# Performance work log

Hardware: AMD Instinct MI355X
Metric: run time of the kernel (lower is better)

The kernel has to match this reference:

```python
import math
import jax, jax.numpy as jnp
import numpy as np

B, H, S, D = 2, 16, 2048, 64


def setup_inputs() -> dict:
    key = jax.random.key(0)
    kq, kk, kv = jax.random.split(key, 3)
    Q = jax.random.normal(kq, (B, H, S, D), dtype=jnp.float32)
    K = jax.random.normal(kk, (B, H, S, D), dtype=jnp.float32)
    V = jax.random.normal(kv, (B, H, S, D), dtype=jnp.float32)
    # padding mask: (N, H, query_len), True = keep (module expands with [..., None])
    padding_mask = jnp.ones((B, H, S), dtype=bool)
    # boolean causal attention mask, broadcastable to (B, H, S, S)
    attention_mask = jnp.tril(jnp.ones((S, S), dtype=bool))[None, None]
    return {"Q": Q, "K": K, "V": V,
            "padding_mask": padding_mask, "attention_mask": attention_mask}


def reference(Q, K, V, padding_mask, attention_mask):
    # scores: (B, H, S_q, S_k)
    scale = 1.0 / math.sqrt(K.shape[-1])
    attn = jnp.einsum("bhqd,bhkd->bhqk", Q, K) * scale
    # query-side padding mask (is_query_mask=True): expand last axis
    attn = jnp.where(padding_mask[..., None], attn, -jnp.inf)
    # boolean attention mask
    attn = jnp.where(attention_mask, attn, -jnp.inf)
    attn = jax.nn.softmax(attn, axis=-1)
    # nan-clean: rows fully masked to -inf softmax to NaN -> 0
    attn = jnp.where(jnp.isnan(attn), 0.0, attn)
    return jnp.einsum("bhqk,bhkd->bhqd", attn, V)
```

## Files before the change

kernel.cpp:

```cpp
#include <hip/hip_runtime.h>


typedef __attribute__((ext_vector_type(8))) short bf16x8;
typedef __attribute__((ext_vector_type(4))) float f32x4;
typedef __attribute__((ext_vector_type(4))) short s16x4;
typedef __attribute__((ext_vector_type(2))) unsigned uint2v;

#define MFMA16(a, b, c) __builtin_amdgcn_mfma_f32_16x16x32_bf16(a, b, c, 0, 0, 0)

#define S_LEN 2048
#define D_DIM 64
#define NBH 32

static __device__ __forceinline__ short f2bf(float f) {
  unsigned u = __builtin_bit_cast(unsigned, f);
  u += 0x7fffu + ((u >> 16) & 1u);
  return (short)(u >> 16);
}

static __device__ __forceinline__ unsigned pk2(float a, float b) {
#if __has_builtin(__builtin_amdgcn_cvt_pk_bf16_f32)
  auto r = __builtin_amdgcn_cvt_pk_bf16_f32(a, b);
  return __builtin_bit_cast(unsigned, r);
#else
  return (unsigned)(unsigned short)f2bf(a) |
         ((unsigned)(unsigned short)f2bf(b) << 16);
#endif
}

static __device__ __forceinline__ float fexp2(float x) {
#if __has_builtin(__builtin_amdgcn_exp2f)
  return __builtin_amdgcn_exp2f(x);
#else
  return exp2f(x);
#endif
}

static __device__ __forceinline__ bf16x8 cvt8(const float* p) {
  f32x4 a = *(const f32x4*)p;
  f32x4 b = *(const f32x4*)(p + 4);
  bf16x8 r;
#pragma unroll
  for (int j = 0; j < 4; ++j) { r[j] = f2bf(a[j]); r[j + 4] = f2bf(b[j]); }
  return r;
}

static __device__ __forceinline__ void load_lds16(const short* g, short* l) {
  __builtin_amdgcn_global_load_lds(
      (const __attribute__((address_space(1))) unsigned*)g,
      (__attribute__((address_space(3))) unsigned*)l, 16, 0, 0);
}

__global__ __launch_bounds__(256) void stage(const float* __restrict__ K,
                                             const float* __restrict__ V,
                                             short* __restrict__ Kb,
                                             short* __restrict__ Vt) {
  const int tid = threadIdx.x;
  if (blockIdx.x < 1024) {
    const size_t b0 = (size_t)blockIdx.x * 4096;
#pragma unroll
    for (int p = 0; p < 2; ++p) {
      const size_t i = b0 + p * 2048 + tid * 8;
      f32x4 a = *(const f32x4*)(K + i);
      f32x4 b = *(const f32x4*)(K + i + 4);
      bf16x8 r;
#pragma unroll
      for (int j = 0; j < 4; ++j) { r[j] = f2bf(a[j]); r[j + 4] = f2bf(b[j]); }
      *(bf16x8*)(Kb + i) = r;
    }
  } else {
    __shared__ unsigned t[64][18];
    const int bi = blockIdx.x - 1024;
    const int bh = bi >> 6, k32 = bi & 63;
    const float* src = V + ((size_t)bh * S_LEN + k32 * 32) * D_DIM;
    const int pr = tid & 15;
    const int dq = tid >> 4;
    f32x4 a = *(const f32x4*)(src + (2 * pr)     * D_DIM + dq * 4);
    f32x4 b = *(const f32x4*)(src + (2 * pr + 1) * D_DIM + dq * 4);
#pragma unroll
    for (int j = 0; j < 4; ++j) t[dq * 4 + j][pr] = pk2(a[j], b[j]);
    __syncthreads();
    const int d = tid >> 2, seg = tid & 3;
    uint2v lo = *(const uint2v*)(&t[d][seg * 4]);
    uint2v hi = *(const uint2v*)(&t[d][seg * 4 + 2]);
    short* dst = Vt + (size_t)bh * D_DIM * S_LEN + (size_t)d * S_LEN +
                 k32 * 32 + seg * 8;
    *(uint2v*)(dst)     = lo;
    *(uint2v*)(dst + 4) = hi;
  }
}

__global__ __launch_bounds__(256, 4) void attn_fwd(
    const float* __restrict__ Q, const short* __restrict__ Kb,
    const short* __restrict__ Vt, float* __restrict__ O) {
  __shared__ __align__(16) short kbuf[2][4096];
  __shared__ __align__(16) short vbuf[2][4096];
  __shared__ __align__(16) short pbuf[4][1024];

  const int tid  = threadIdx.x;
  const int wave = tid >> 6;
  const int lane = tid & 63;
  const int quad = lane >> 4;
  const int col  = lane & 15;

  const int bh = blockIdx.x & 31;
  const int qb = 31 - (blockIdx.x >> 5);
  const int n  = qb + 1;
  const int q0 = qb * 64 + wave * 16;

  const float* Qh = Q  + (size_t)bh * S_LEN * D_DIM;
  const short* Kh = Kb + (size_t)bh * S_LEN * D_DIM;
  const short* Vh = Vt + (size_t)bh * D_DIM * S_LEN;

  const bf16x8 bq0 = cvt8(Qh + (q0 + col) * D_DIM + quad * 8);
  const bf16x8 bq1 = cvt8(Qh + (q0 + col) * D_DIM + quad * 8 + 32);

  const int L0 = tid,       r0s = L0 >> 3, c0s = (L0 & 7) ^ (r0s & 7);
  const int L1 = 256 + tid, r1s = L1 >> 3, c1s = (L1 & 7) ^ (r1s & 7);
  const int wb0 = (wave * 64) * 8;
  const int wb1 = (256 + wave * 64) * 8;

  f32x4 o[4];
#pragma unroll
  for (int i = 0; i < 4; ++i) o[i] = 0.f;
  float psum = 0.f;
  const float sc = 0.125f * 1.44269504088896340736f;

  const int rbase = col * 64;
  const int sw0 = ((quad       ^ (col & 7)) << 3);
  const int sw1 = (((4 + quad) ^ (col & 7)) << 3);
  short* pw = &pbuf[wave][col * 64];
  const int cw0 = (quad >> 1), ho = (quad & 1) << 2;

  auto prefetch = [&](int t, int buf) {
    const int k0n = t << 6;
    load_lds16(Kh + (size_t)(k0n + r0s) * 64 + c0s * 8, &kbuf[buf][wb0]);
    load_lds16(Kh + (size_t)(k0n + r1s) * 64 + c1s * 8, &kbuf[buf][wb1]);
    load_lds16(Vh + (size_t)r0s * S_LEN + k0n + c0s * 8, &vbuf[buf][wb0]);
    load_lds16(Vh + (size_t)r1s * S_LEN + k0n + c1s * 8, &vbuf[buf][wb1]);
  };

  auto body = [&](int t, bool masked) {
    const short* kb = kbuf[t & 1];
    const short* vb = vbuf[t & 1];

    bf16x8 av0[4], av1[4];
#pragma unroll
    for (int mt = 0; mt < 4; ++mt) {
      av0[mt] = *(const bf16x8*)(vb + mt * 1024 + rbase + sw0);
      av1[mt] = *(const bf16x8*)(vb + mt * 1024 + rbase + sw1);
    }

    f32x4 s[4];
#pragma unroll
    for (int mt = 0; mt < 4; ++mt) {
      bf16x8 a0 = *(const bf16x8*)(kb + mt * 1024 + rbase + sw0);
      bf16x8 a1 = *(const bf16x8*)(kb + mt * 1024 + rbase + sw1);
      f32x4 c = 0.f;
      c = MFMA16(a0, bq0, c);
      c = MFMA16(a1, bq1, c);
      s[mt] = c;
    }

    const int k0 = t << 6, qA = q0 + col;
#pragma unroll
    for (int mt = 0; mt < 4; ++mt) {
      float p0 = fexp2(fmaf(s[mt][0], sc, -8.0f));
      float p1 = fexp2(fmaf(s[mt][1], sc, -8.0f));
      float p2 = fexp2(fmaf(s[mt][2], sc, -8.0f));
      float p3 = fexp2(fmaf(s[mt][3], sc, -8.0f));
      if (masked) {
        const int kk = k0 + mt * 16 + quad * 4;
        if (kk     > qA) p0 = 0.f;
        if (kk + 1 > qA) p1 = 0.f;
        if (kk + 2 > qA) p2 = 0.f;
        if (kk + 3 > qA) p3 = 0.f;
      }
      psum += (p0 + p1) + (p2 + p3);
      uint2v u; u[0] = pk2(p0, p1); u[1] = pk2(p2, p3);
      *(uint2v*)(pw + (((2 * mt + cw0) ^ (col & 7)) << 3) + ho) = u;
    }

#pragma unroll
    for (int h = 0; h < 2; ++h) {
      const bf16x8 bp = *(const bf16x8*)(pw + (((h * 4 + quad) ^ (col & 7)) << 3));
#pragma unroll
      for (int mt = 0; mt < 4; ++mt)
        o[mt] = MFMA16(h ? av1[mt] : av0[mt], bp, o[mt]);
    }
  };

  prefetch(0, 0);
  for (int t = 0; t < n - 1; ++t) {
    __syncthreads();
    prefetch(t + 1, (t + 1) & 1);
    body(t, false);
  }
  __syncthreads();
  body(n - 1, true);

  psum += __shfl_xor(psum, 16);
  psum += __shfl_xor(psum, 32);
  const float rl = 1.f / psum;
  float* op = O + (size_t)bh * S_LEN * D_DIM + (size_t)(q0 + col) * D_DIM;
#pragma unroll
  for (int mt = 0; mt < 4; ++mt) {
    f32x4 ov;
#pragma unroll
    for (int r = 0; r < 4; ++r) ov[r] = o[mt][r] * rl;
    *(f32x4*)(op + mt * 16 + quad * 4) = ov;
  }
}

extern "C" void kernel_launch(void* const* d_in, const int* in_sizes, int n_in,
                              void* d_out, int out_size, void* d_ws, size_t ws_size,
                              hipStream_t stream) {
  const float* Q = (const float*)d_in[0];
  const float* K = (const float*)d_in[1];
  const float* V = (const float*)d_in[2];
  short* Kb = (short*)d_ws;
  short* Vt = Kb + (size_t)NBH * S_LEN * D_DIM;
  stage   <<<dim3(3072), dim3(256), 0, stream>>>(K, V, Kb, Vt);
  attn_fwd<<<dim3(1024), dim3(256), 0, stream>>>(Q, Kb, Vt, (float*)d_out);
}
```

Before: 141.5 us.

## Fuse K/V bf16 conversion and V transpose into attention kernel loads

Drops the separate staging kernel that converted K to bf16 and wrote a transposed bf16 V to workspace. The attention kernel now loads fp32 K/V tiles into registers, runs the current tile's compute, then converts, transposes and writes the next tile into swizzled LDS. This removes a kernel launch and the workspace round trip. In exchange each block redoes the conversion for every tile it touches, reads twice the bytes in fp32, and gives up the async global-to-LDS loads, which adds register pressure at 4 waves/SIMD occupancy.

```diff
diff --git a/kernel.cpp b/kernel.cpp
--- a/kernel.cpp
+++ b/kernel.cpp
@@ -3,7 +3,6 @@
 
 typedef __attribute__((ext_vector_type(8))) short bf16x8;
 typedef __attribute__((ext_vector_type(4))) float f32x4;
-typedef __attribute__((ext_vector_type(4))) short s16x4;
 typedef __attribute__((ext_vector_type(2))) unsigned uint2v;
 
 #define MFMA16(a, b, c) __builtin_amdgcn_mfma_f32_16x16x32_bf16(a, b, c, 0, 0, 0)
@@ -45,54 +44,14 @@
   return r;
 }
 
-static __device__ __forceinline__ void load_lds16(const short* g, short* l) {
-  __builtin_amdgcn_global_load_lds(
-      (const __attribute__((address_space(1))) unsigned*)g,
-      (__attribute__((address_space(3))) unsigned*)l, 16, 0, 0);
-}
-
-__global__ __launch_bounds__(256) void stage(const float* __restrict__ K,
-                                             const float* __restrict__ V,
-                                             short* __restrict__ Kb,
-                                             short* __restrict__ Vt) {
-  const int tid = threadIdx.x;
-  if (blockIdx.x < 1024) {
-    const size_t b0 = (size_t)blockIdx.x * 4096;
-#pragma unroll
-    for (int p = 0; p < 2; ++p) {
-      const size_t i = b0 + p * 2048 + tid * 8;
-      f32x4 a = *(const f32x4*)(K + i);
-      f32x4 b = *(const f32x4*)(K + i + 4);
-      bf16x8 r;
-#pragma unroll
-      for (int j = 0; j < 4; ++j) { r[j] = f2bf(a[j]); r[j + 4] = f2bf(b[j]); }
-      *(bf16x8*)(Kb + i) = r;
-    }
-  } else {
-    __shared__ unsigned t[64][18];
-    const int bi = blockIdx.x - 1024;
-    const int bh = bi >> 6, k32 = bi & 63;
-    const float* src = V + ((size_t)bh * S_LEN + k32 * 32) * D_DIM;
-    const int pr = tid & 15;
-    const int dq = tid >> 4;
-    f32x4 a = *(const f32x4*)(src + (2 * pr)     * D_DIM + dq * 4);
-    f32x4 b = *(const f32x4*)(src + (2 * pr + 1) * D_DIM + dq * 4);
-#pragma unroll
-    for (int j = 0; j < 4; ++j) t[dq * 4 + j][pr] = pk2(a[j], b[j]);
-    __syncthreads();
-    const int d = tid >> 2, seg = tid & 3;
-    uint2v lo = *(const uint2v*)(&t[d][seg * 4]);
-    uint2v hi = *(const uint2v*)(&t[d][seg * 4 + 2]);
-    short* dst = Vt + (size_t)bh * D_DIM * S_LEN + (size_t)d * S_LEN +
-                 k32 * 32 + seg * 8;
-    *(uint2v*)(dst)     = lo;
-    *(uint2v*)(dst + 4) = hi;
-  }
-}
+struct StageRegs {
+  f32x4 ka[4];
+  f32x4 va0, va1, vb0, vb1;
+};
 
 __global__ __launch_bounds__(256, 4) void attn_fwd(
-    const float* __restrict__ Q, const short* __restrict__ Kb,
-    const short* __restrict__ Vt, float* __restrict__ O) {
+    const float* __restrict__ Q, const float* __restrict__ K,
+    const float* __restrict__ V, float* __restrict__ O) {
   __shared__ __align__(16) short kbuf[2][4096];
   __shared__ __align__(16) short vbuf[2][4096];
   __shared__ __align__(16) short pbuf[4][1024];
@@ -108,17 +67,17 @@
   const int n  = qb + 1;
   const int q0 = qb * 64 + wave * 16;
 
-  const float* Qh = Q  + (size_t)bh * S_LEN * D_DIM;
-  const short* Kh = Kb + (size_t)bh * S_LEN * D_DIM;
-  const short* Vh = Vt + (size_t)bh * D_DIM * S_LEN;
+  const float* Qh = Q + (size_t)bh * S_LEN * D_DIM;
+  const float* Kh = K + (size_t)bh * S_LEN * D_DIM;
+  const float* Vh = V + (size_t)bh * S_LEN * D_DIM;
 
   const bf16x8 bq0 = cvt8(Qh + (q0 + col) * D_DIM + quad * 8);
   const bf16x8 bq1 = cvt8(Qh + (q0 + col) * D_DIM + quad * 8 + 32);
 
-  const int L0 = tid,       r0s = L0 >> 3, c0s = (L0 & 7) ^ (r0s & 7);
-  const int L1 = 256 + tid, r1s = L1 >> 3, c1s = (L1 & 7) ^ (r1s & 7);
-  const int wb0 = (wave * 64) * 8;
-  const int wb1 = (256 + wave * 64) * 8;
+  const int kwa = (tid >> 4) * 64 +
+                  (((((tid & 15) >> 1)) ^ ((tid >> 4) & 7)) << 3) +
+                  4 * (tid & 1);
+  const int pr = tid & 31, dq = tid >> 5;
 
   f32x4 o[4];
 #pragma unroll
@@ -132,12 +91,36 @@
   short* pw = &pbuf[wave][col * 64];
   const int cw0 = (quad >> 1), ho = (quad & 1) << 2;
 
-  auto prefetch = [&](int t, int buf) {
-    const int k0n = t << 6;
-    load_lds16(Kh + (size_t)(k0n + r0s) * 64 + c0s * 8, &kbuf[buf][wb0]);
-    load_lds16(Kh + (size_t)(k0n + r1s) * 64 + c1s * 8, &kbuf[buf][wb1]);
-    load_lds16(Vh + (size_t)r0s * S_LEN + k0n + c0s * 8, &vbuf[buf][wb0]);
-    load_lds16(Vh + (size_t)r1s * S_LEN + k0n + c1s * 8, &vbuf[buf][wb1]);
+  auto load_tile = [&](int t) {
+    StageRegs r;
+    const float* kp = Kh + (size_t)(t << 6) * D_DIM;
+    const float* vp = Vh + (size_t)(t << 6) * D_DIM;
+#pragma unroll
+    for (int p = 0; p < 4; ++p)
+      r.ka[p] = *(const f32x4*)(kp + p * 1024 + tid * 4);
+    r.va0 = *(const f32x4*)(vp + (2 * pr) * D_DIM + 8 * dq);
+    r.va1 = *(const f32x4*)(vp + (2 * pr) * D_DIM + 8 * dq + 4);
+    r.vb0 = *(const f32x4*)(vp + (2 * pr + 1) * D_DIM + 8 * dq);
+    r.vb1 = *(const f32x4*)(vp + (2 * pr + 1) * D_DIM + 8 * dq + 4);
+    return r;
+  };
+
+  auto write_tile = [&](const StageRegs& r, int buf) {
+#pragma unroll
+    for (int p = 0; p < 4; ++p) {
+      uint2v u;
+      u[0] = pk2(r.ka[p][0], r.ka[p][1]);
+      u[1] = pk2(r.ka[p][2], r.ka[p][3]);
+      *(uint2v*)(&kbuf[buf][p * 1024 + kwa]) = u;
+    }
+    unsigned* vb = (unsigned*)&vbuf[buf][0];
+#pragma unroll
+    for (int j = 0; j < 4; ++j) {
+      vb[(8 * dq + j) * 32 + (((pr >> 2) ^ j) << 2) + (pr & 3)] =
+          pk2(r.va0[j], r.vb0[j]);
+      vb[(8 * dq + 4 + j) * 32 + (((pr >> 2) ^ (4 + j)) << 2) + (pr & 3)] =
+          pk2(r.va1[j], r.vb1[j]);
+    }
   };
 
   auto body = [&](int t, bool masked) {
@@ -190,11 +173,16 @@
     }
   };
 
-  prefetch(0, 0);
+  {
+    StageRegs r0 = load_tile(0);
+    write_tile(r0, 0);
+  }
+
   for (int t = 0; t < n - 1; ++t) {
     __syncthreads();
-    prefetch(t + 1, (t + 1) & 1);
+    StageRegs r = load_tile(t + 1);
     body(t, false);
+    write_tile(r, (t + 1) & 1);
   }
   __syncthreads();
   body(n - 1, true);
@@ -218,8 +206,5 @@
   const float* Q = (const float*)d_in[0];
   const float* K = (const float*)d_in[1];
   const float* V = (const float*)d_in[2];
-  short* Kb = (short*)d_ws;
-  short* Vt = Kb + (size_t)NBH * S_LEN * D_DIM;
-  stage   <<<dim3(3072), dim3(256), 0, stream>>>(K, V, Kb, Vt);
-  attn_fwd<<<dim3(1024), dim3(256), 0, stream>>>(Q, Kb, Vt, (float*)d_out);
-}
+  attn_fwd<<<dim3(1024), dim3(256), 0, stream>>>(Q, K, V, (float*)d_out);
+}
```

Result: slower. 145.4 us (+2.8%).

## Split key tile across waves and reduce partial outputs through LDS

Applied to the files above, without the earlier changes.

Each wave now handles 16 keys of the 64-key tile against all 64 queries, instead of 16 queries against all keys. The P matrix then stays in registers and feeds 16x16x16 MFMAs directly, removing the per-wave P round trip through LDS. Each wave keeps partial 64x64 outputs and row sums, which are merged by a multi-step LDS tree reduction at the end. The cost is 64 accumulator registers per lane, occupancy lowered to 3 waves per SIMD, extra synchronization and a serial epilogue, and the half-width MFMA for PV.

```diff
diff --git a/kernel.cpp b/kernel.cpp
--- a/kernel.cpp
+++ b/kernel.cpp
@@ -2,11 +2,11 @@
 
 
 typedef __attribute__((ext_vector_type(8))) short bf16x8;
+typedef __attribute__((ext_vector_type(4))) short bf16x4;
 typedef __attribute__((ext_vector_type(4))) float f32x4;
-typedef __attribute__((ext_vector_type(4))) short s16x4;
 typedef __attribute__((ext_vector_type(2))) unsigned uint2v;
 
-#define MFMA16(a, b, c) __builtin_amdgcn_mfma_f32_16x16x32_bf16(a, b, c, 0, 0, 0)
+#define MFMA32(a, b, c) __builtin_amdgcn_mfma_f32_16x16x32_bf16(a, b, c, 0, 0, 0)
 
 #define S_LEN 2048
 #define D_DIM 64
@@ -33,6 +33,18 @@
   return __builtin_amdgcn_exp2f(x);
 #else
   return exp2f(x);
+#endif
+}
+
+static __device__ __forceinline__ f32x4 mfma16(bf16x4 a, bf16x4 b, f32x4 c) {
+#if __has_builtin(__builtin_amdgcn_mfma_f32_16x16x16_bf16)
+  return __builtin_amdgcn_mfma_f32_16x16x16_bf16(a, b, c, 0, 0, 0);
+#elif __has_builtin(__builtin_amdgcn_mfma_f32_16x16x16bf16_1k)
+  return __builtin_amdgcn_mfma_f32_16x16x16bf16_1k(a, b, c, 0, 0, 0);
+#else
+  bf16x8 a8 = {a[0], a[1], a[2], a[3], 0, 0, 0, 0};
+  bf16x8 b8 = {b[0], b[1], b[2], b[3], 0, 0, 0, 0};
+  return MFMA32(a8, b8, c);
 #endif
 }
 
@@ -90,12 +102,14 @@
   }
 }
 
-__global__ __launch_bounds__(256, 4) void attn_fwd(
+__global__ __launch_bounds__(256, 3) void attn_fwd(
     const float* __restrict__ Q, const short* __restrict__ Kb,
     const short* __restrict__ Vt, float* __restrict__ O) {
   __shared__ __align__(16) short kbuf[2][4096];
   __shared__ __align__(16) short vbuf[2][4096];
-  __shared__ __align__(16) short pbuf[4][1024];
+  __shared__ float lbuf[4][64];
+  float* regA = (float*)&kbuf[0][0];
+  float* regB = (float*)&vbuf[0][0];
 
   const int tid  = threadIdx.x;
   const int wave = tid >> 6;
@@ -106,31 +120,37 @@
   const int bh = blockIdx.x & 31;
   const int qb = 31 - (blockIdx.x >> 5);
   const int n  = qb + 1;
-  const int q0 = qb * 64 + wave * 16;
+  const int q0 = qb * 64;
 
   const float* Qh = Q  + (size_t)bh * S_LEN * D_DIM;
   const short* Kh = Kb + (size_t)bh * S_LEN * D_DIM;
   const short* Vh = Vt + (size_t)bh * D_DIM * S_LEN;
 
-  const bf16x8 bq0 = cvt8(Qh + (q0 + col) * D_DIM + quad * 8);
-  const bf16x8 bq1 = cvt8(Qh + (q0 + col) * D_DIM + quad * 8 + 32);
+  bf16x8 bq[4][2];
+#pragma unroll
+  for (int nt = 0; nt < 4; ++nt) {
+    bq[nt][0] = cvt8(Qh + (q0 + nt * 16 + col) * D_DIM + quad * 8);
+    bq[nt][1] = cvt8(Qh + (q0 + nt * 16 + col) * D_DIM + quad * 8 + 32);
+  }
 
   const int L0 = tid,       r0s = L0 >> 3, c0s = (L0 & 7) ^ (r0s & 7);
   const int L1 = 256 + tid, r1s = L1 >> 3, c1s = (L1 & 7) ^ (r1s & 7);
   const int wb0 = (wave * 64) * 8;
   const int wb1 = (256 + wave * 64) * 8;
 
-  f32x4 o[4];
-#pragma unroll
-  for (int i = 0; i < 4; ++i) o[i] = 0.f;
-  float psum = 0.f;
-  const float sc = 0.125f * 1.44269504088896340736f;
-
-  const int rbase = col * 64;
+  const int krbase = (wave * 16 + col) * 64;
   const int sw0 = ((quad       ^ (col & 7)) << 3);
   const int sw1 = (((4 + quad) ^ (col & 7)) << 3);
-  short* pw = &pbuf[wave][col * 64];
-  const int cw0 = (quad >> 1), ho = (quad & 1) << 2;
+  const int vsw = (((2 * wave + (quad >> 1)) ^ (col & 7)) << 3) +
+                  ((quad & 1) << 2);
+
+  f32x4 o[4][4];
+#pragma unroll
+  for (int i = 0; i < 4; ++i)
+#pragma unroll
+    for (int j = 0; j < 4; ++j) o[i][j] = 0.f;
+  float ps[4] = {0.f, 0.f, 0.f, 0.f};
+  const float sc = 0.125f * 1.44269504088896340736f;
 
   auto prefetch = [&](int t, int buf) {
     const int k0n = t << 6;
@@ -144,49 +164,40 @@
     const short* kb = kbuf[t & 1];
     const short* vb = vbuf[t & 1];
 
-    bf16x8 av0[4], av1[4];
-#pragma unroll
-    for (int mt = 0; mt < 4; ++mt) {
-      av0[mt] = *(const bf16x8*)(vb + mt * 1024 + rbase + sw0);
-      av1[mt] = *(const bf16x8*)(vb + mt * 1024 + rbase + sw1);
-    }
-
-    f32x4 s[4];
-#pragma unroll
-    for (int mt = 0; mt < 4; ++mt) {
-      bf16x8 a0 = *(const bf16x8*)(kb + mt * 1024 + rbase + sw0);
-      bf16x8 a1 = *(const bf16x8*)(kb + mt * 1024 + rbase + sw1);
-      f32x4 c = 0.f;
-      c = MFMA16(a0, bq0, c);
-      c = MFMA16(a1, bq1, c);
-      s[mt] = c;
-    }
-
-    const int k0 = t << 6, qA = q0 + col;
-#pragma unroll
-    for (int mt = 0; mt < 4; ++mt) {
-      float p0 = fexp2(fmaf(s[mt][0], sc, -8.0f));
-      float p1 = fexp2(fmaf(s[mt][1], sc, -8.0f));
-      float p2 = fexp2(fmaf(s[mt][2], sc, -8.0f));
-      float p3 = fexp2(fmaf(s[mt][3], sc, -8.0f));
+    bf16x4 av[4];
+#pragma unroll
+    for (int mt = 0; mt < 4; ++mt)
+      av[mt] = *(const bf16x4*)(vb + (mt * 16 + col) * 64 + vsw);
+
+    const bf16x8 a0 = *(const bf16x8*)(kb + krbase + sw0);
+    const bf16x8 a1 = *(const bf16x8*)(kb + krbase + sw1);
+
+#pragma unroll
+    for (int nt = 0; nt < 4; ++nt) {
+      f32x4 s = 0.f;
+      s = MFMA32(a0, bq[nt][0], s);
+      s = MFMA32(a1, bq[nt][1], s);
+
+      float p0 = fexp2(fmaf(s[0], sc, -8.0f));
+      float p1 = fexp2(fmaf(s[1], sc, -8.0f));
+      float p2 = fexp2(fmaf(s[2], sc, -8.0f));
+      float p3 = fexp2(fmaf(s[3], sc, -8.0f));
       if (masked) {
-        const int kk = k0 + mt * 16 + quad * 4;
-        if (kk     > qA) p0 = 0.f;
-        if (kk + 1 > qA) p1 = 0.f;
-        if (kk + 2 > qA) p2 = 0.f;
-        if (kk + 3 > qA) p3 = 0.f;
-      }
-      psum += (p0 + p1) + (p2 + p3);
+        const int kk = wave * 16 + quad * 4;
+        const int qq = nt * 16 + col;
+        if (kk     > qq) p0 = 0.f;
+        if (kk + 1 > qq) p1 = 0.f;
+        if (kk + 2 > qq) p2 = 0.f;
+        if (kk + 3 > qq) p3 = 0.f;
+      }
+      ps[nt] += (p0 + p1) + (p2 + p3);
+
       uint2v u; u[0] = pk2(p0, p1); u[1] = pk2(p2, p3);
-      *(uint2v*)(pw + (((2 * mt + cw0) ^ (col & 7)) << 3) + ho) = u;
-    }
-
-#pragma unroll
-    for (int h = 0; h < 2; ++h) {
-      const bf16x8 bp = *(const bf16x8*)(pw + (((h * 4 + quad) ^ (col & 7)) << 3));
+      const bf16x4 pb = __builtin_bit_cast(bf16x4, u);
+
 #pragma unroll
       for (int mt = 0; mt < 4; ++mt)
-        o[mt] = MFMA16(h ? av1[mt] : av0[mt], bp, o[mt]);
+        o[mt][nt] = mfma16(av[mt], pb, o[mt][nt]);
     }
   };
 
@@ -199,16 +210,67 @@
   __syncthreads();
   body(n - 1, true);
 
-  psum += __shfl_xor(psum, 16);
-  psum += __shfl_xor(psum, 32);
-  const float rl = 1.f / psum;
-  float* op = O + (size_t)bh * S_LEN * D_DIM + (size_t)(q0 + col) * D_DIM;
-#pragma unroll
-  for (int mt = 0; mt < 4; ++mt) {
-    f32x4 ov;
-#pragma unroll
-    for (int r = 0; r < 4; ++r) ov[r] = o[mt][r] * rl;
-    *(f32x4*)(op + mt * 16 + quad * 4) = ov;
+#pragma unroll
+  for (int nt = 0; nt < 4; ++nt) {
+    ps[nt] += __shfl_xor(ps[nt], 16);
+    ps[nt] += __shfl_xor(ps[nt], 32);
+  }
+  if (quad == 0) {
+#pragma unroll
+    for (int nt = 0; nt < 4; ++nt) lbuf[wave][nt * 16 + col] = ps[nt];
+  }
+
+  auto wr = [&](float* reg) {
+#pragma unroll
+    for (int mt = 0; mt < 4; ++mt)
+#pragma unroll
+      for (int nt = 0; nt < 4; ++nt) {
+        const int q = nt * 16 + col, c = mt * 4 + quad;
+        const int pos = (c & 8) | ((c & 7) ^ (q & 7));
+        *(f32x4*)(reg + q * 64 + pos * 4) = o[mt][nt];
+      }
+  };
+  auto rd = [&](const float* reg) {
+#pragma unroll
+    for (int mt = 0; mt < 4; ++mt)
+#pragma unroll
+      for (int nt = 0; nt < 4; ++nt) {
+        const int q = nt * 16 + col, c = mt * 4 + quad;
+        const int pos = (c & 8) | ((c & 7) ^ (q & 7));
+        const f32x4 v = *(const f32x4*)(reg + q * 64 + pos * 4);
+#pragma unroll
+        for (int r = 0; r < 4; ++r) o[mt][nt][r] += v[r];
+      }
+  };
+
+  __syncthreads();
+  if (wave == 2) wr(regA);
+  if (wave == 3) wr(regB);
+  __syncthreads();
+  if (wave == 0) rd(regA);
+  if (wave == 1) rd(regB);
+  __syncthreads();
+  if (wave == 1) wr(regA);
+  __syncthreads();
+  if (wave == 0) {
+    rd(regA);
+    float rl[4];
+#pragma unroll
+    for (int nt = 0; nt < 4; ++nt) {
+      const int q = nt * 16 + col;
+      rl[nt] = 1.f / (lbuf[0][q] + lbuf[1][q] + lbuf[2][q] + lbuf[3][q]);
+    }
+    float* op = O + (size_t)bh * S_LEN * D_DIM;
+#pragma unroll
+    for (int mt = 0; mt < 4; ++mt)
+#pragma unroll
+      for (int nt = 0; nt < 4; ++nt) {
+        f32x4 ov;
+#pragma unroll
+        for (int r = 0; r < 4; ++r) ov[r] = o[mt][nt][r] * rl[nt];
+        *(f32x4*)(op + (size_t)(q0 + nt * 16 + col) * D_DIM +
+                  mt * 16 + quad * 4) = ov;
+      }
   }
 }
 
```

After: 145.9 us. +3.1%, slower.
